# Optimization experiments

Measured on AMD Instinct MI355X. Metric: run time of the kernel, lower is better.

## Reference

```python
import jax, jax.numpy as jnp
import numpy as np

EPS = 1e-5
B, M, N, D = 8, 4096, 1024, 1024


def setup_inputs() -> dict:
    key = jax.random.key(0)
    kx, kw, kb, kg, kbe = jax.random.split(key, 5)
    return {
        "x": jax.random.normal(kx, (B, M, N), dtype=jnp.float32),
        "w": jax.random.normal(kw, (N, D), dtype=jnp.float32) * 0.02,
        "b": jax.random.normal(kb, (D,), dtype=jnp.float32) * 0.02,
        "gamma": jax.random.uniform(kg, (N,), dtype=jnp.float32, minval=0.5, maxval=1.5),
        "beta": jax.random.normal(kbe, (N,), dtype=jnp.float32) * 0.02,
    }


def reference(x, w, b, gamma, beta):
    # Fused LayerNorm (over last dim, biased variance, eps=1e-5) + matmul + bias.
    mean = jnp.mean(x, axis=-1, keepdims=True)                 # [B,M,1]
    var = jnp.mean(jnp.square(x - mean), axis=-1, keepdims=True)
    rstd = jax.lax.rsqrt(var + EPS)                            # [B,M,1]
    ln = (x - mean) * rstd * gamma + beta                      # [B,M,N]
    return jnp.einsum('bmn,nd->bmd', ln, w) + b                # [B,M,D]
```

## Files before the change

### kernel.cpp

```cpp
#include <hip/hip_runtime.h>
#include <stdint.h>

#define RROWS 32768
#define KDIM  1024
#define DDIM  1024

typedef __bf16 bf16;
typedef __bf16 bf16x4 __attribute__((ext_vector_type(4)));
typedef __bf16 bf16x8 __attribute__((ext_vector_type(8)));
typedef float  f32x4  __attribute__((ext_vector_type(4)));

typedef __attribute__((address_space(1))) const unsigned int* gas_ptr;
typedef __attribute__((address_space(3))) unsigned int* las_ptr;

__global__ __launch_bounds__(256) void prep_gt(const float* __restrict__ w,
                                               const float* __restrict__ gamma,
                                               bf16* __restrict__ Gt) {
    __shared__ float tile[64][65];
    const int k0 = blockIdx.x * 64;
    const int d0 = blockIdx.y * 64;
    const int t  = threadIdx.x;
    const int col4 = (t & 15) * 4;
    const int rowb = t >> 4;
#pragma unroll
    for (int r = 0; r < 4; ++r) {
        const int k = rowb + r * 16;
        const float4 v = *(const float4*)&w[(size_t)(k0 + k) * DDIM + d0 + col4];
        const float g = gamma[k0 + k];
        tile[k][col4 + 0] = v.x * g;
        tile[k][col4 + 1] = v.y * g;
        tile[k][col4 + 2] = v.z * g;
        tile[k][col4 + 3] = v.w * g;
    }
    __syncthreads();
#pragma unroll
    for (int r = 0; r < 2; ++r) {
        const int d  = (t >> 3) + r * 32;
        const int ks = (t & 7) * 8;
        bf16x8 o;
#pragma unroll
        for (int j = 0; j < 8; ++j) o[j] = (bf16)tile[ks + j][d];
        *(bf16x8*)&Gt[(size_t)(d0 + d) * KDIM + k0 + ks] = o;
    }
}

__global__ __launch_bounds__(256) void prep_part(const float* __restrict__ w,
                                                 const float* __restrict__ gamma,
                                                 const float* __restrict__ beta,
                                                 float* __restrict__ partG,
                                                 float* __restrict__ partB) {
    const int d  = blockIdx.x * 256 + threadIdx.x;
    const int kc = blockIdx.y;
    float ag = 0.f, ab = 0.f;
    for (int k = kc * 64; k < kc * 64 + 64; ++k) {
        const float wv = w[(size_t)k * DDIM + d];
        ag += gamma[k] * wv;
        ab += beta[k] * wv;
    }
    partG[(size_t)kc * DDIM + d] = ag;
    partB[(size_t)kc * DDIM + d] = ab;
}

__global__ __launch_bounds__(256) void prep_reduce(const float* __restrict__ partG,
                                                   const float* __restrict__ partB,
                                                   const float* __restrict__ b,
                                                   float* __restrict__ gw,
                                                   float* __restrict__ cvec) {
    const int d = blockIdx.x * 256 + threadIdx.x;
    float g = 0.f, a = 0.f;
#pragma unroll
    for (int j = 0; j < 16; ++j) {
        g += partG[(size_t)j * DDIM + d];
        a += partB[(size_t)j * DDIM + d];
    }
    gw[d]   = g;
    cvec[d] = a + b[d];
}

__global__ __launch_bounds__(256) void ln_convert(const float* __restrict__ x,
                                                  bf16* __restrict__ xb) {
    const int wave = threadIdx.x >> 6;
    const int lane = threadIdx.x & 63;
    const int row  = blockIdx.x * 4 + wave;
    const float4* xr = (const float4*)(x + (size_t)row * KDIM);

    float4 v[4];
    float s1 = 0.f, s2 = 0.f;
#pragma unroll
    for (int j = 0; j < 4; ++j) {
        v[j] = xr[lane + j * 64];
        s1 += v[j].x + v[j].y + v[j].z + v[j].w;
        s2 += v[j].x * v[j].x + v[j].y * v[j].y + v[j].z * v[j].z + v[j].w * v[j].w;
    }
#pragma unroll
    for (int ofs = 1; ofs < 64; ofs <<= 1) {
        s1 += __shfl_xor(s1, ofs, 64);
        s2 += __shfl_xor(s2, ofs, 64);
    }
    const float mean = s1 * (1.0f / KDIM);
    const float var  = s2 * (1.0f / KDIM) - mean * mean;
    const float rstd = rsqrtf(var + 1e-5f);

    bf16x4* xo = (bf16x4*)(xb + (size_t)row * KDIM);
#pragma unroll
    for (int j = 0; j < 4; ++j) {
        bf16x4 o;
        o[0] = (bf16)((v[j].x - mean) * rstd);
        o[1] = (bf16)((v[j].y - mean) * rstd);
        o[2] = (bf16)((v[j].z - mean) * rstd);
        o[3] = (bf16)((v[j].w - mean) * rstd);
        xo[lane + j * 64] = o;
    }
}

#define BM 128
#define BN 128
#define BK 64

__global__ __launch_bounds__(256) void gemm_bt(const bf16* __restrict__ xb,
                                               const bf16* __restrict__ Gt,
                                               const float* __restrict__ cvec,
                                               float* __restrict__ out) {
    __shared__ __align__(16) bf16 As[BM * BK];
    __shared__ __align__(16) bf16 Bs[BN * BK];

    const int t     = threadIdx.x;
    const int dTile = blockIdx.x;
    const int mTile = blockIdx.y;
    const int row0  = mTile * BM;
    const int col0  = dTile * BN;

    const int wave = t >> 6;
    const int lane = t & 63;
    const int wr   = wave >> 1;
    const int wc   = wave & 1;
    const int quad = lane >> 4;
    const int r16  = lane & 15;

    f32x4 acc[4][4];
#pragma unroll
    for (int i = 0; i < 4; ++i)
#pragma unroll
        for (int j = 0; j < 4; ++j) acc[i][j] = (f32x4)0.0f;

    for (int k0 = 0; k0 < KDIM; k0 += BK) {
        __syncthreads();

#pragma unroll
        for (int j = 0; j < 4; ++j) {
            const int ci   = j * 256 + t;
            const int row  = ci >> 3;
            const int slot = ci & 7;
            const int q    = slot ^ (row & 7);
            const bf16* gp = xb + (size_t)(row0 + row) * KDIM + k0 + q * 8;
            char* lp = (char*)As + ci * 16;
            __builtin_amdgcn_global_load_lds((gas_ptr)(const void*)gp,
                                             (las_ptr)(void*)lp, 16, 0, 0);
        }
#pragma unroll
        for (int j = 0; j < 4; ++j) {
            const int ci   = j * 256 + t;
            const int row  = ci >> 3;
            const int slot = ci & 7;
            const int q    = slot ^ (row & 7);
            const bf16* gp = Gt + (size_t)(col0 + row) * KDIM + k0 + q * 8;
            char* lp = (char*)Bs + ci * 16;
            __builtin_amdgcn_global_load_lds((gas_ptr)(const void*)gp,
                                             (las_ptr)(void*)lp, 16, 0, 0);
        }

        __syncthreads();

#pragma unroll
        for (int kk = 0; kk < 2; ++kk) {
            bf16x8 af[4], bfr[4];
#pragma unroll
            for (int i = 0; i < 4; ++i) {
                const int row  = wr * 64 + i * 16 + r16;
                const int slot = (kk * 4 + quad) ^ (row & 7);
                af[i] = *(const bf16x8*)&As[row * BK + slot * 8];
            }
#pragma unroll
            for (int j = 0; j < 4; ++j) {
                const int row  = wc * 64 + j * 16 + r16;
                const int slot = (kk * 4 + quad) ^ (row & 7);
                bfr[j] = *(const bf16x8*)&Bs[row * BK + slot * 8];
            }
#pragma unroll
            for (int i = 0; i < 4; ++i)
#pragma unroll
                for (int j = 0; j < 4; ++j)
                    acc[i][j] = __builtin_amdgcn_mfma_f32_16x16x32_bf16(af[i], bfr[j], acc[i][j], 0, 0, 0);
        }
    }

    const int lr = quad * 4;
    const int lc = r16;
#pragma unroll
    for (int j = 0; j < 4; ++j) {
        const int col = col0 + wc * 64 + j * 16 + lc;
        const float cv = cvec[col];
#pragma unroll
        for (int i = 0; i < 4; ++i) {
#pragma unroll
            for (int rg = 0; rg < 4; ++rg) {
                const int row = row0 + wr * 64 + i * 16 + lr + rg;
                out[(size_t)row * DDIM + col] = acc[i][j][rg] + cv;
            }
        }
    }
}

#define FBK 32
#define APAD 40

__global__ __launch_bounds__(256) void fused_gemm(const float* __restrict__ x,
                                                  const bf16* __restrict__ Gt,
                                                  const float* __restrict__ gw,
                                                  const float* __restrict__ cvec,
                                                  float* __restrict__ out) {
    __shared__ __align__(16) bf16 As2[BM * APAD];
    __shared__ __align__(16) bf16 Bs2[BM * FBK];
    __shared__ float meanS[BM];
    __shared__ float rstdS[BM];

    const int t     = threadIdx.x;
    const int mTile = blockIdx.x;
    const int dTile = blockIdx.y;
    const int row0  = mTile * BM;
    const int col0  = dTile * BN;
    const int wave = t >> 6;
    const int lane = t & 63;
    const int wr   = wave >> 1;
    const int wc   = wave & 1;
    const int a_row = t >> 3;
    const int a_seg = t & 7;

    float s1[4] = {0.f, 0.f, 0.f, 0.f};
    float s2[4] = {0.f, 0.f, 0.f, 0.f};
    f32x4 acc[4][4];
#pragma unroll
    for (int i = 0; i < 4; ++i)
#pragma unroll
        for (int j = 0; j < 4; ++j) acc[i][j] = (f32x4)0.0f;

    for (int k0 = 0; k0 < KDIM; k0 += FBK) {
        __syncthreads();
#pragma unroll
        for (int j = 0; j < 2; ++j) {
            const int off  = j * 4096 + t * 16;
            const int brow = off >> 6;
            const int kseg = (off & 63) >> 1;
            const bf16* gp = Gt + (size_t)(col0 + brow) * KDIM + k0 + kseg;
            char* lp = (char*)Bs2 + off;
            __builtin_amdgcn_global_load_lds((gas_ptr)(const void*)gp,
                                             (las_ptr)(void*)lp, 16, 0, 0);
        }
#pragma unroll
        for (int r = 0; r < 4; ++r) {
            const int row = r * 32 + a_row;
            const float4 v = *(const float4*)&x[(size_t)(row0 + row) * KDIM + k0 + a_seg * 4];
            s1[r] += v.x + v.y + v.z + v.w;
            s2[r] += v.x * v.x + v.y * v.y + v.z * v.z + v.w * v.w;
            bf16x4 pk;
            pk[0] = (bf16)v.x; pk[1] = (bf16)v.y; pk[2] = (bf16)v.z; pk[3] = (bf16)v.w;
            *(bf16x4*)&As2[row * APAD + a_seg * 4] = pk;
        }
        __syncthreads();

        bf16x8 af[4], bfr[4];
        const int arow = wr * 64 + (lane & 15);
        const int brow = wc * 64 + (lane & 15);
        const int koff = (lane >> 4) * 8;
#pragma unroll
        for (int i = 0; i < 4; ++i)
            af[i] = *(const bf16x8*)&As2[(arow + i * 16) * APAD + koff];
#pragma unroll
        for (int j = 0; j < 4; ++j)
            bfr[j] = *(const bf16x8*)&Bs2[(brow + j * 16) * FBK + koff];
#pragma unroll
        for (int i = 0; i < 4; ++i)
#pragma unroll
            for (int j = 0; j < 4; ++j)
                acc[i][j] = __builtin_amdgcn_mfma_f32_16x16x32_bf16(af[i], bfr[j], acc[i][j], 0, 0, 0);
    }

#pragma unroll
    for (int r = 0; r < 4; ++r) {
        float a = s1[r], b = s2[r];
#pragma unroll
        for (int ofs = 1; ofs < 8; ofs <<= 1) {
            a += __shfl_xor(a, ofs, 64);
            b += __shfl_xor(b, ofs, 64);
        }
        if (a_seg == 0) {
            const int row = r * 32 + a_row;
            const float mean = a * (1.0f / KDIM);
            const float var  = b * (1.0f / KDIM) - mean * mean;
            meanS[row] = mean;
            rstdS[row] = rsqrtf(var + 1e-5f);
        }
    }
    __syncthreads();

    const int lr = (lane >> 4) * 4;
    const int lc = lane & 15;
#pragma unroll
    for (int j = 0; j < 4; ++j) {
        const int col = col0 + wc * 64 + j * 16 + lc;
        const float gwv = gw[col];
        const float cv  = cvec[col];
#pragma unroll
        for (int i = 0; i < 4; ++i) {
#pragma unroll
            for (int rg = 0; rg < 4; ++rg) {
                const int rowL = wr * 64 + i * 16 + lr + rg;
                const float vv = rstdS[rowL] * (acc[i][j][rg] - meanS[rowL] * gwv) + cv;
                out[(size_t)(row0 + rowL) * DDIM + col] = vv;
            }
        }
    }
}

extern "C" void kernel_launch(void* const* d_in, const int* in_sizes, int n_in,
                              void* d_out, int out_size, void* d_ws, size_t ws_size,
                              hipStream_t stream) {
    const float* x     = (const float*)d_in[0];
    const float* w     = (const float*)d_in[1];
    const float* b     = (const float*)d_in[2];
    const float* gamma = (const float*)d_in[3];
    const float* beta  = (const float*)d_in[4];
    float* out = (float*)d_out;

    char* ws = (char*)d_ws;
    const size_t XB_B = (size_t)RROWS * KDIM * sizeof(bf16);
    bf16*  xb    = (bf16*)ws;
    bf16*  Gt    = (bf16*)(ws + XB_B);
    float* partG = (float*)(ws + XB_B + (2u << 20));
    float* partB = (float*)(ws + XB_B + (2u << 20) + (64u << 10));
    float* gw    = (float*)(ws + XB_B + (2u << 20) + (128u << 10));
    float* cvec  = (float*)(ws + XB_B + (2u << 20) + (132u << 10));

    const bool big_ws = ws_size >= XB_B + (3u << 20);

    if (big_ws) {
        prep_gt<<<dim3(16, 16), 256, 0, stream>>>(w, gamma, Gt);
        prep_part<<<dim3(4, 16), 256, 0, stream>>>(w, gamma, beta, partG, partB);
        prep_reduce<<<4, 256, 0, stream>>>(partG, partB, b, gw, cvec);
        ln_convert<<<RROWS / 4, 256, 0, stream>>>(x, xb);
        gemm_bt<<<dim3(8, 256), 256, 0, stream>>>(xb, Gt, cvec, out);
    } else {
        bf16*  Gt2    = (bf16*)ws;
        float* partG2 = (float*)(ws + (2u << 20));
        float* partB2 = (float*)(ws + (2u << 20) + (64u << 10));
        float* gw2    = (float*)(ws + (2u << 20) + (128u << 10));
        float* cvec2  = (float*)(ws + (2u << 20) + (132u << 10));
        prep_gt<<<dim3(16, 16), 256, 0, stream>>>(w, gamma, Gt2);
        prep_part<<<dim3(4, 16), 256, 0, stream>>>(w, gamma, beta, partG2, partB2);
        prep_reduce<<<4, 256, 0, stream>>>(partG2, partB2, b, gw2, cvec2);
        fused_gemm<<<dim3(256, 8), 256, 0, stream>>>(x, Gt2, gw2, cvec2, out);
    }
}
```

Measured before the change: 339.1 us.

## Double-buffer LDS tiles in bf16 GEMM with BK=32 and swap grid order

The GEMM main loop now uses two LDS buffers with a K-tile of 32, issuing global-to-LDS loads for the next tile before computing the current one, so memory latency overlaps with MFMA work and one barrier per iteration is removed. The grid is also transposed so consecutive blocks walk along M for a fixed D tile, which changes L2 reuse of the weight matrix versus the activation rows. The smaller K-tile doubles the number of iterations and barriers and gives less MFMA work per barrier. There is also no explicit wait on outstanding async LDS loads beyond __syncthreads, so correctness relies on the compiler inserting the vmcnt waits.

```diff
diff --git a/kernel.cpp b/kernel.cpp
--- a/kernel.cpp
+++ b/kernel.cpp
@@ -115,18 +115,19 @@
 
 #define BM 128
 #define BN 128
-#define BK 64
+#define BK 32
+#define NK (KDIM / BK)
 
 __global__ __launch_bounds__(256) void gemm_bt(const bf16* __restrict__ xb,
                                                const bf16* __restrict__ Gt,
                                                const float* __restrict__ cvec,
                                                float* __restrict__ out) {
-    __shared__ __align__(16) bf16 As[BM * BK];
-    __shared__ __align__(16) bf16 Bs[BN * BK];
+    __shared__ __align__(16) bf16 As[2][BM * BK];
+    __shared__ __align__(16) bf16 Bs[2][BN * BK];
 
     const int t     = threadIdx.x;
-    const int dTile = blockIdx.x;
-    const int mTile = blockIdx.y;
+    const int mTile = blockIdx.x;
+    const int dTile = blockIdx.y;
     const int row0  = mTile * BM;
     const int col0  = dTile * BN;
 
@@ -137,62 +138,61 @@
     const int quad = lane >> 4;
     const int r16  = lane & 15;
 
+    const int ci0 = t;
+    const int ci1 = 256 + t;
+
     f32x4 acc[4][4];
 #pragma unroll
     for (int i = 0; i < 4; ++i)
 #pragma unroll
         for (int j = 0; j < 4; ++j) acc[i][j] = (f32x4)0.0f;
 
-    for (int k0 = 0; k0 < KDIM; k0 += BK) {
+    auto stage = [&](int buf, int k0) {
+#pragma unroll
+        for (int j = 0; j < 2; ++j) {
+            const int ci   = j ? ci1 : ci0;
+            const int row  = ci >> 2;
+            const int slot = ci & 3;
+            const int q    = slot ^ (row & 3);
+            const bf16* ga = xb + (size_t)(row0 + row) * KDIM + k0 + q * 8;
+            const bf16* gb = Gt + (size_t)(col0 + row) * KDIM + k0 + q * 8;
+            __builtin_amdgcn_global_load_lds((gas_ptr)(const void*)ga,
+                                             (las_ptr)(void*)((char*)&As[buf][0] + ci * 16), 16, 0, 0);
+            __builtin_amdgcn_global_load_lds((gas_ptr)(const void*)gb,
+                                             (las_ptr)(void*)((char*)&Bs[buf][0] + ci * 16), 16, 0, 0);
+        }
+    };
+
+    auto compute = [&](int buf) {
+        bf16x8 af[4], bfr[4];
+#pragma unroll
+        for (int i = 0; i < 4; ++i) {
+            const int row  = wr * 64 + i * 16 + r16;
+            const int slot = quad ^ (row & 3);
+            af[i] = *(const bf16x8*)&As[buf][row * BK + slot * 8];
+        }
+#pragma unroll
+        for (int j = 0; j < 4; ++j) {
+            const int row  = wc * 64 + j * 16 + r16;
+            const int slot = quad ^ (row & 3);
+            bfr[j] = *(const bf16x8*)&Bs[buf][row * BK + slot * 8];
+        }
+#pragma unroll
+        for (int i = 0; i < 4; ++i)
+#pragma unroll
+            for (int j = 0; j < 4; ++j)
+                acc[i][j] = __builtin_amdgcn_mfma_f32_16x16x32_bf16(af[i], bfr[j], acc[i][j], 0, 0, 0);
+    };
+
+    stage(0, 0);
+#pragma unroll 1
+    for (int it = 0; it < NK - 1; ++it) {
         __syncthreads();
-
-#pragma unroll
-        for (int j = 0; j < 4; ++j) {
-            const int ci   = j * 256 + t;
-            const int row  = ci >> 3;
-            const int slot = ci & 7;
-            const int q    = slot ^ (row & 7);
-            const bf16* gp = xb + (size_t)(row0 + row) * KDIM + k0 + q * 8;
-            char* lp = (char*)As + ci * 16;
-            __builtin_amdgcn_global_load_lds((gas_ptr)(const void*)gp,
-                                             (las_ptr)(void*)lp, 16, 0, 0);
-        }
-#pragma unroll
-        for (int j = 0; j < 4; ++j) {
-            const int ci   = j * 256 + t;
-            const int row  = ci >> 3;
-            const int slot = ci & 7;
-            const int q    = slot ^ (row & 7);
-            const bf16* gp = Gt + (size_t)(col0 + row) * KDIM + k0 + q * 8;
-            char* lp = (char*)Bs + ci * 16;
-            __builtin_amdgcn_global_load_lds((gas_ptr)(const void*)gp,
-                                             (las_ptr)(void*)lp, 16, 0, 0);
-        }
-
-        __syncthreads();
-
-#pragma unroll
-        for (int kk = 0; kk < 2; ++kk) {
-            bf16x8 af[4], bfr[4];
-#pragma unroll
-            for (int i = 0; i < 4; ++i) {
-                const int row  = wr * 64 + i * 16 + r16;
-                const int slot = (kk * 4 + quad) ^ (row & 7);
-                af[i] = *(const bf16x8*)&As[row * BK + slot * 8];
-            }
-#pragma unroll
-            for (int j = 0; j < 4; ++j) {
-                const int row  = wc * 64 + j * 16 + r16;
-                const int slot = (kk * 4 + quad) ^ (row & 7);
-                bfr[j] = *(const bf16x8*)&Bs[row * BK + slot * 8];
-            }
-#pragma unroll
-            for (int i = 0; i < 4; ++i)
-#pragma unroll
-                for (int j = 0; j < 4; ++j)
-                    acc[i][j] = __builtin_amdgcn_mfma_f32_16x16x32_bf16(af[i], bfr[j], acc[i][j], 0, 0, 0);
-        }
-    }
+        stage((it + 1) & 1, (it + 1) * BK);
+        compute(it & 1);
+    }
+    __syncthreads();
+    compute((NK - 1) & 1);
 
     const int lr = quad * 4;
     const int lc = r16;
@@ -348,7 +348,7 @@
         prep_part<<<dim3(4, 16), 256, 0, stream>>>(w, gamma, beta, partG, partB);
         prep_reduce<<<4, 256, 0, stream>>>(partG, partB, b, gw, cvec);
         ln_convert<<<RROWS / 4, 256, 0, stream>>>(x, xb);
-        gemm_bt<<<dim3(8, 256), 256, 0, stream>>>(xb, Gt, cvec, out);
+        gemm_bt<<<dim3(256, 8), 256, 0, stream>>>(xb, Gt, cvec, out);
     } else {
         bf16*  Gt2    = (bf16*)ws;
         float* partG2 = (float*)(ws + (2u << 20));
```

New measurement: 355.5 us. +4.8%, slower.
